# Kernel optimization log

Hardware: AMD Instinct MI355X
Metric: run time of the kernel (lower is better)

## Reference

```python
import jax, jax.numpy as jnp
import numpy as np
from functools import partial

B, A_PER, FH, FW, STRIDE = 32, 9, 100, 100, 16
PRE_NMS = 1000
POST_NMS = 1000
NMS_THRESH = 0.7
SCORE_THRESH = 0.0
MIN_SIZE = 0.001
BBOX_CLIP = float(np.log(1000.0 / 16.0))  # torchvision decode clamp on dw, dh


def make_anchors():
    # 3 scales x 3 ratios = 9 base anchors, tiled over the stride-16 grid in (h, w, a) order
    scales = np.array([32.0, 64.0, 128.0])
    ratios = np.array([0.5, 1.0, 2.0])
    ws = (scales[:, None] / np.sqrt(ratios)[None, :]).reshape(-1)
    hs = (scales[:, None] * np.sqrt(ratios)[None, :]).reshape(-1)
    base = np.stack([-ws / 2, -hs / 2, ws / 2, hs / 2], axis=1)  # [9,4]
    sx = (np.arange(FW) + 0.5) * STRIDE
    sy = (np.arange(FH) + 0.5) * STRIDE
    gy, gx = np.meshgrid(sy, sx, indexing="ij")
    shifts = np.stack([gx, gy, gx, gy], axis=-1)  # [H,W,4]
    anc = shifts[:, :, None, :] + base[None, None, :, :]  # [H,W,9,4]
    return jnp.asarray(anc.reshape(-1, 4), dtype=jnp.float32)


def setup_inputs() -> dict:
    key = jax.random.key(0)
    k1, k2 = jax.random.split(key)
    objectness = jax.random.normal(k1, (B, A_PER, FH, FW), dtype=jnp.float32)
    bbox_deltas = jax.random.normal(k2, (B, 4 * A_PER, FH, FW), dtype=jnp.float32)
    anchors = make_anchors()  # [FH*FW*A_PER, 4]
    return {"objectness": objectness, "bbox_deltas": bbox_deltas,
            "anchors": anchors, "image_h": FH * STRIDE, "image_w": FW * STRIDE}


def _flatten_head(cls, deltas):
    # cls: [B, A, H, W] (C=1); deltas: [B, 4A, H, W] -> (h, w, a) anchor order
    b, a, h, w = cls.shape
    obj = cls.transpose(0, 2, 3, 1).reshape(b, -1)                      # [B, HW*A]
    d = deltas.reshape(b, a, 4, h, w).transpose(0, 3, 4, 1, 2).reshape(b, -1, 4)
    return obj, d


def _decode(deltas, anchors):
    aw = anchors[:, 2] - anchors[:, 0]
    ah = anchors[:, 3] - anchors[:, 1]
    acx = anchors[:, 0] + 0.5 * aw
    acy = anchors[:, 1] + 0.5 * ah
    dx, dy = deltas[..., 0], deltas[..., 1]
    dw = jnp.minimum(deltas[..., 2], BBOX_CLIP)
    dh = jnp.minimum(deltas[..., 3], BBOX_CLIP)
    pcx = dx * aw + acx
    pcy = dy * ah + acy
    pw = jnp.exp(dw) * aw
    ph = jnp.exp(dh) * ah
    return jnp.stack([pcx - 0.5 * pw, pcy - 0.5 * ph,
                      pcx + 0.5 * pw, pcy + 0.5 * ph], axis=-1)


def _box_iou(a, b):
    area_a = (a[:, 2] - a[:, 0]) * (a[:, 3] - a[:, 1])
    area_b = (b[:, 2] - b[:, 0]) * (b[:, 3] - b[:, 1])
    lt = jnp.maximum(a[:, None, :2], b[None, :, :2])
    rb = jnp.minimum(a[:, None, 2:], b[None, :, 2:])
    wh = jnp.maximum(rb - lt, 0.0)
    inter = wh[..., 0] * wh[..., 1]
    return inter / (area_a[:, None] + area_b[None, :] - inter + 1e-12)


def _nms_keep(boxes, valid):
    # greedy NMS over score-sorted boxes; `valid` pre-masks small/low-score boxes
    k = boxes.shape[0]
    iou = _box_iou(boxes, boxes)
    ar = jnp.arange(k)

    def body(i, keep):
        sup = (iou[i] > NMS_THRESH) & keep[i] & (ar > i)
        return keep & jnp.logical_not(sup)

    return jax.lax.fori_loop(0, k, body, valid)


def _filter_one(boxes, logits, img_h, img_w):
    # boxes: [A,4], logits: [A]; per-image top-k -> clip -> filters -> NMS -> post top-k
    scores, idx = jax.lax.top_k(logits, PRE_NMS)     # sorted descending
    boxes = boxes[idx]
    prob = jax.nn.sigmoid(jax.lax.stop_gradient(scores))  # objectness is detached in filter_proposals
    x1 = jnp.clip(boxes[:, 0], 0.0, float(img_w))
    y1 = jnp.clip(boxes[:, 1], 0.0, float(img_h))
    x2 = jnp.clip(boxes[:, 2], 0.0, float(img_w))
    y2 = jnp.clip(boxes[:, 3], 0.0, float(img_h))
    boxes = jnp.stack([x1, y1, x2, y2], axis=-1)
    ws = boxes[:, 2] - boxes[:, 0]
    hs = boxes[:, 3] - boxes[:, 1]
    valid = (ws >= MIN_SIZE) & (hs >= MIN_SIZE) & (prob >= SCORE_THRESH)
    keep = jax.lax.stop_gradient(_nms_keep(boxes, valid))
    order = jnp.argsort(jnp.where(keep, 0, 1))[:POST_NMS]  # stable: kept boxes first, score order
    m = keep[order]
    out_boxes = jnp.where(m[:, None], boxes[order], 0.0)
    out_prob = jnp.where(m, prob[order], 0.0)
    return out_boxes, out_prob, m


def reference(objectness, bbox_deltas, anchors, image_h, image_w):
    obj, d = _flatten_head(objectness, bbox_deltas)      # [B, A_tot], [B, A_tot, 4]
    proposals = _decode(d, anchors)                      # [B, A_tot, 4]
    f = partial(_filter_one, img_h=image_h, img_w=image_w)
    boxes, prob, mask = jax.vmap(f)(proposals, obj)      # [B, POST_NMS, 4], [B, POST_NMS], [B, POST_NMS]
    return boxes, prob, mask
```

## Files before the change

kernel.cpp:

```cpp
#include <hip/hip_runtime.h>
#include <math.h>

#define BATCH 32
#define A_PER 9
#define FH 100
#define FW 100
#define A_TOT (FH*FW*A_PER)
#define KSEL 1000
#define BUFCAP 2048
#define NBIN 4096
#define NMS_T 0.7f
#define MIN_SZ 0.001f
#define BBOX_CLIP_F 4.135166556742356f

__device__ __forceinline__ unsigned int f2key(float f) {
    unsigned int u = __float_as_uint(f);
    return u ^ ((u & 0x80000000u) ? 0xFFFFFFFFu : 0x80000000u);
}
__device__ __forceinline__ float key2f(unsigned int k) {
    return __uint_as_float((k & 0x80000000u) ? (k ^ 0x80000000u) : ~k);
}

__global__ __launch_bounds__(256) void zero_kernel(
    uint4* __restrict__ ghist4, uint4* __restrict__ gcand4,
    uint4* __restrict__ gcnt4, uint4* __restrict__ valid4)
{
    const uint4 z = make_uint4(0u, 0u, 0u, 0u);
    int bid = blockIdx.x;
    if (bid < 128) {
        ghist4[bid * 256 + threadIdx.x] = z;
    } else if (bid < 256) {
        gcand4[(bid - 128) * 256 + threadIdx.x] = z;
    } else if (bid == 256) {
        if (threadIdx.x < 8) gcnt4[threadIdx.x] = z;
    } else {
        valid4[threadIdx.x] = z;
    }
}

__global__ __launch_bounds__(256) void hist_kernel(
    const float* __restrict__ obj, unsigned int* __restrict__ ghist)
{
    const int b = blockIdx.x >> 4;
    const int part = blockIdx.x & 15;
    const int tid = threadIdx.x;
    __shared__ unsigned int h[NBIN];
    for (int i = tid; i < NBIN; i += 256) h[i] = 0u;
    __syncthreads();
    const float4* sc4 = (const float4*)(obj + (size_t)b * A_TOT);
    for (int i = part * 256 + tid; i < A_TOT / 4; i += 4096) {
        float4 v = sc4[i];
        atomicAdd(&h[f2key(v.x) >> 20], 1u);
        atomicAdd(&h[f2key(v.y) >> 20], 1u);
        atomicAdd(&h[f2key(v.z) >> 20], 1u);
        atomicAdd(&h[f2key(v.w) >> 20], 1u);
    }
    __syncthreads();
    unsigned int* gh = ghist + (size_t)b * NBIN;
    for (int i = tid; i < NBIN; i += 256)
        if (h[i]) atomicAdd(&gh[i], h[i]);
}

__global__ __launch_bounds__(1024) void gather_kernel(
    const float* __restrict__ obj, const unsigned int* __restrict__ ghist,
    unsigned long long* __restrict__ gcand, unsigned int* __restrict__ gcnt)
{
    const int b = blockIdx.x >> 3;
    const int part = blockIdx.x & 7;
    const int tid = threadIdx.x;
    const int lane = tid & 63;
    const int wv = tid >> 6;

    __shared__ unsigned int wsum[16];
    __shared__ unsigned int sh_T, lcnt, base_sh;
    __shared__ unsigned long long cbuf[BUFCAP];

    if (tid == 0) lcnt = 0u;

    const unsigned int* gh = ghist + (size_t)b * NBIN;
    unsigned int h0 = gh[tid * 4 + 0], h1 = gh[tid * 4 + 1];
    unsigned int h2 = gh[tid * 4 + 2], h3 = gh[tid * 4 + 3];
    unsigned int ts = h0 + h1 + h2 + h3;
    unsigned int x = ts;
#pragma unroll
    for (int off = 1; off < 64; off <<= 1) {
        unsigned int v = __shfl_down(x, off);
        if (lane + off < 64) x += v;
    }
    if (lane == 0) wsum[wv] = x;
    __syncthreads();
    unsigned int swave = 0;
    for (int q = wv + 1; q < 16; ++q) swave += wsum[q];
    unsigned int S_hi = swave + (x - ts);
    unsigned int a3 = S_hi;
    unsigned int a2 = a3 + h3;
    unsigned int a1 = a2 + h2;
    unsigned int a0 = a1 + h1;
    if (a3 < KSEL && a3 + h3 >= KSEL) sh_T = (unsigned)(tid * 4 + 3);
    if (a2 < KSEL && a2 + h2 >= KSEL) sh_T = (unsigned)(tid * 4 + 2);
    if (a1 < KSEL && a1 + h1 >= KSEL) sh_T = (unsigned)(tid * 4 + 1);
    if (a0 < KSEL && a0 + h0 >= KSEL) sh_T = (unsigned)(tid * 4 + 0);
    __syncthreads();
    unsigned int T = sh_T;

    const float4* sc4 = (const float4*)(obj + (size_t)b * A_TOT);
#pragma unroll
    for (int j = 0; j < 3; ++j) {
        int i4 = j * 8192 + part * 1024 + tid;
        if (i4 < A_TOT / 4) {
            float4 v = sc4[i4];
            float vs[4] = {v.x, v.y, v.z, v.w};
#pragma unroll
            for (int c = 0; c < 4; ++c) {
                unsigned int key = f2key(vs[c]);
                if ((key >> 20) >= T) {
                    unsigned int pos = atomicAdd(&lcnt, 1u);
                    if (pos < BUFCAP) {
                        int e = i4 * 4 + c;
                        int a = e / 10000; int rem = e - a * 10000;
                        unsigned int i = (unsigned int)(rem * 9 + a);
                        cbuf[pos] = ((unsigned long long)key << 32) | (unsigned int)(~i);
                    }
                }
            }
        }
    }
    __syncthreads();
    if (tid == 0) base_sh = atomicAdd(&gcnt[b], lcnt);
    __syncthreads();
    unsigned int base = base_sh, n = lcnt;
    for (unsigned int i = tid; i < n; i += 1024) {
        unsigned int p = base + i;
        if (p < BUFCAP) gcand[(size_t)b * BUFCAP + p] = cbuf[i];
    }
}

__global__ __launch_bounds__(256) void rank_decode_kernel(
    const float* __restrict__ deltas,
    const float* __restrict__ anchors,
    const int* __restrict__ imh_p, const int* __restrict__ imw_p,
    const unsigned long long* __restrict__ gcand,
    const unsigned int* __restrict__ gcnt,
    float* __restrict__ boxes_ws, float* __restrict__ prob_ws,
    unsigned long long* __restrict__ valid_ws)
{
    const int b = blockIdx.x >> 3;
    const int part = blockIdx.x & 7;
    const int tid = threadIdx.x;
    const int lane = tid & 63;

    unsigned int cnt = gcnt[b]; if (cnt > BUFCAP) cnt = BUFCAP;
    const unsigned long long* gc = gcand + (size_t)b * BUFCAP;
    const int c = part * 256 + tid;
    unsigned long long my = gc[c];
    bool active = (c < (int)cnt);

    unsigned int ntile = (cnt + 63u) >> 6;
    unsigned int rank = 0;
    for (unsigned int t0 = 0; t0 < ntile; ++t0) {
        unsigned long long kk = gc[t0 * 64 + lane];
        unsigned int lo = (unsigned int)kk, hi = (unsigned int)(kk >> 32);
#pragma unroll
        for (int t = 0; t < 64; ++t) {
            unsigned int khi = __builtin_amdgcn_readlane(hi, t);
            unsigned int klo = __builtin_amdgcn_readlane(lo, t);
            unsigned long long kj = ((unsigned long long)khi << 32) | klo;
            rank += (kj > my) ? 1u : 0u;
        }
    }

    if (active && rank < KSEL) {
        unsigned int keyhi = (unsigned int)(my >> 32);
        unsigned int i = ~((unsigned int)my);
        float score = key2f(keyhi);
        float prob = 1.0f / (1.0f + expf(-score));

        int a = (int)(i % 9u); int hw = (int)(i / 9u);
        int h = hw / 100, w = hw - 100 * (hw / 100);
        const float* D = deltas + (size_t)b * 36 * 10000;
        int off = h * 100 + w;
        float dx  = D[(a * 4 + 0) * 10000 + off];
        float dy  = D[(a * 4 + 1) * 10000 + off];
        float dwv = fminf(D[(a * 4 + 2) * 10000 + off], BBOX_CLIP_F);
        float dhv = fminf(D[(a * 4 + 3) * 10000 + off], BBOX_CLIP_F);
        const float* anc = anchors + (size_t)i * 4;
        float ax1 = anc[0], ay1 = anc[1], ax2 = anc[2], ay2 = anc[3];
        float aw = ax2 - ax1, ah = ay2 - ay1;
        float acx = ax1 + 0.5f * aw, acy = ay1 + 0.5f * ah;
        float pcx = dx * aw + acx, pcy = dy * ah + acy;
        float pw = expf(dwv) * aw, ph = expf(dhv) * ah;
        float imw = (float)(*imw_p);
        float imh = (float)(*imh_p);
        float x1 = pcx - 0.5f * pw, y1 = pcy - 0.5f * ph;
        float x2 = pcx + 0.5f * pw, y2 = pcy + 0.5f * ph;
        x1 = fminf(fmaxf(x1, 0.0f), imw);
        y1 = fminf(fmaxf(y1, 0.0f), imh);
        x2 = fminf(fmaxf(x2, 0.0f), imw);
        y2 = fminf(fmaxf(y2, 0.0f), imh);
        bool valid = ((x2 - x1) >= MIN_SZ) && ((y2 - y1) >= MIN_SZ) && (prob >= 0.0f);
        ((float4*)boxes_ws)[(size_t)b * KSEL + rank] = make_float4(x1, y1, x2, y2);
        prob_ws[(size_t)b * KSEL + rank] = prob;
        if (valid)
            atomicOr(&valid_ws[b * 16 + (rank >> 6)], 1ull << (rank & 63));
    }
}

__global__ __launch_bounds__(1024) void mask_kernel(
    const float* __restrict__ boxes_ws, unsigned long long* __restrict__ mask_ws)
{
    const int b = blockIdx.x >> 3;
    const int part = blockIdx.x & 7;
    const int tid = threadIdx.x;
    const int lane = tid & 63;
    const int wv = tid >> 6;
    __shared__ float4 bx[KSEL];
    __shared__ float ar[KSEL];
    for (int r = tid; r < KSEL; r += 1024) {
        float4 v = ((const float4*)boxes_ws)[(size_t)b * KSEL + r];
        bx[r] = v;
        ar[r] = (v.z - v.x) * (v.w - v.y);
    }
    __syncthreads();
    int slot = part * 16 + wv;
    for (int r = slot; r < KSEL; r += 128) {
        float4 a = bx[r];
        float area_a = ar[r];
        unsigned long long* row = mask_ws + ((size_t)b * KSEL + r) * 16;
        int wlo = r >> 6;
        for (int t = 0; t < 16; ++t) {
            if (t < wlo) { if (lane == 0) row[t] = 0ull; continue; }
            int j = (t << 6) | lane;
            bool bit = false;
            if (j > r && j < KSEL) {
                float4 c = bx[j];
                float xx1 = fmaxf(a.x, c.x), yy1 = fmaxf(a.y, c.y);
                float xx2 = fminf(a.z, c.z), yy2 = fminf(a.w, c.w);
                float iw = fmaxf(xx2 - xx1, 0.0f), ih = fmaxf(yy2 - yy1, 0.0f);
                float inter = iw * ih;
                float iou = inter / (area_a + ar[j] - inter + 1e-12f);
                bit = iou > NMS_T;
            }
            unsigned long long m = __ballot(bit ? 1 : 0);
            if (lane == 0) row[t] = m;
        }
    }
}

__global__ __launch_bounds__(1024) void nms_out_kernel(
    const float* __restrict__ boxes_ws, const float* __restrict__ prob_ws,
    const unsigned long long* __restrict__ valid_ws,
    const unsigned long long* __restrict__ mask_ws,
    float* __restrict__ out)
{
    const int b = blockIdx.x;
    const int tid = threadIdx.x;
    const int lane = tid & 63;
    const int wv = tid >> 6;

    __shared__ unsigned long long partial[16];
    __shared__ unsigned long long keepw_sh[16];
    __shared__ unsigned int psum[16];
    __shared__ int klist[1024];
    __shared__ int cnt_sh;

    const unsigned long long* M = mask_ws + (size_t)b * KSEL * 16;

    unsigned long long Dd[16];
    unsigned long long validw = 0ull;
    if (wv == 0) {
#pragma unroll
        for (int w = 0; w < 16; ++w) {
            int row = w * 64 + lane;
            Dd[w] = (row < KSEL) ? M[(size_t)row * 16 + w] : 0ull;
        }
        validw = (lane < 16) ? valid_ws[b * 16 + lane] : 0ull;
    }
    if (tid == 0) { cnt_sh = 0; klist[0] = 0; }
    __syncthreads();

#pragma unroll
    for (int w = 0; w < 16; ++w) {
        int cnt = cnt_sh;
        int j = wv * 64 + lane;
        int jj = (j < cnt) ? j : 0;
        int kidx = klist[jj];
        unsigned long long v = M[(size_t)kidx * 16 + w];
        if (j >= cnt) v = 0ull;
#pragma unroll
        for (int off = 32; off > 0; off >>= 1) v |= __shfl_xor(v, off);
        if (lane == 0) partial[wv] = v;
        __syncthreads();

        if (wv == 0) {
            unsigned long long sup = (lane < 16) ? partial[lane] : 0ull;
#pragma unroll
            for (int off = 32; off > 0; off >>= 1) sup |= __shfl_xor(sup, off);
            unsigned long long cw = __shfl(validw, w) & ~sup;
            unsigned long long Dw = Dd[w];
            unsigned long long keptw = 0ull;
            while (cw) {
                unsigned long long myrow = Dw & cw;
                unsigned long long confl =
                    __ballot((((cw >> lane) & 1ull) && myrow != 0ull) ? 1 : 0);
                if (confl == 0ull) { keptw |= cw; break; }
                int c = __ffsll((long long)confl) - 1;
                unsigned long long le = (c == 63) ? ~0ull : ((1ull << (c + 1)) - 1ull);
                keptw |= cw & le;
                unsigned long long Dc = __shfl(Dw, c);
                cw &= ~le & ~Dc;
            }
            if ((keptw >> lane) & 1ull) {
                int rank = (int)__popcll(keptw & ((1ull << lane) - 1ull));
                klist[cnt + rank] = w * 64 + lane;
            }
            if (lane == 0) {
                keepw_sh[w] = keptw;
                cnt_sh = cnt + (int)__popcll(keptw);
            }
        }
        __syncthreads();
    }

    if (tid == 0) {
        unsigned int s = 0;
        for (int wq = 0; wq < 16; ++wq) { psum[wq] = s; s += __popcll(keepw_sh[wq]); }
    }
    __syncthreads();

    float* ob = out;
    float* op = out + (size_t)BATCH * KSEL * 4;
    float* om = op + (size_t)BATCH * KSEL;
    float* obb = ob + (size_t)b * KSEL * 4;
    float* opb = op + (size_t)b * KSEL;
    float* omb = om + (size_t)b * KSEL;

    for (int r = tid; r < KSEL; r += 1024) {
        obb[r * 4 + 0] = 0.0f; obb[r * 4 + 1] = 0.0f;
        obb[r * 4 + 2] = 0.0f; obb[r * 4 + 3] = 0.0f;
        opb[r] = 0.0f; omb[r] = 0.0f;
    }
    __syncthreads();
    for (int r = tid; r < KSEL; r += 1024) {
        unsigned long long kw = keepw_sh[r >> 6];
        if ((kw >> (r & 63)) & 1ull) {
            unsigned int p = psum[r >> 6] + (unsigned int)__popcll(kw & ((1ull << (r & 63)) - 1ull));
            size_t src = ((size_t)b * KSEL + r) * 4;
            obb[p * 4 + 0] = boxes_ws[src + 0];
            obb[p * 4 + 1] = boxes_ws[src + 1];
            obb[p * 4 + 2] = boxes_ws[src + 2];
            obb[p * 4 + 3] = boxes_ws[src + 3];
            opb[p] = prob_ws[(size_t)b * KSEL + r];
            omb[p] = 1.0f;
        }
    }
}

extern "C" void kernel_launch(void* const* d_in, const int* in_sizes, int n_in,
                              void* d_out, int out_size, void* d_ws, size_t ws_size,
                              hipStream_t stream) {
    const float* obj     = (const float*)d_in[0];
    const float* deltas  = (const float*)d_in[1];
    const float* anchors = (const float*)d_in[2];
    const int*   imh     = (const int*)d_in[3];
    const int*   imw     = (const int*)d_in[4];
    float* out = (float*)d_out;

    char* ws = (char*)d_ws;
    float* boxes_ws = (float*)ws;
    float* prob_ws  = (float*)(ws + 512000);
    unsigned long long* valid_ws = (unsigned long long*)(ws + 640000);
    unsigned long long* mask_ws  = (unsigned long long*)(ws + 644096);
    unsigned int* ghist = (unsigned int*)(ws + 644096);
    unsigned long long* gcand = (unsigned long long*)(ws + 1168384);
    unsigned int* gcnt  = (unsigned int*)(ws + 1692672);

    zero_kernel<<<258, 256, 0, stream>>>((uint4*)ghist, (uint4*)gcand,
                                         (uint4*)gcnt, (uint4*)valid_ws);
    hist_kernel<<<BATCH * 16, 256, 0, stream>>>(obj, ghist);
    gather_kernel<<<BATCH * 8, 1024, 0, stream>>>(obj, ghist, gcand, gcnt);
    rank_decode_kernel<<<BATCH * 8, 256, 0, stream>>>(deltas, anchors, imh, imw,
                                                      gcand, gcnt, boxes_ws, prob_ws, valid_ws);
    mask_kernel<<<BATCH * 8, 1024, 0, stream>>>(boxes_ws, mask_ws);
    nms_out_kernel<<<BATCH, 1024, 0, stream>>>(boxes_ws, prob_ws, valid_ws, mask_ws, out);
}
```

Before: 175.9 us.

## Fuse rank, decode, IoU mask and NMS into one per-image kernel

Removes the zero kernel by writing per-partition histograms and candidate lists that need no atomics or clearing. Rank, decode, IoU mask and NMS are merged into a single block per image that keeps boxes in shared memory. Suppression masks are now built lazily: only the diagonal 64x64 blocks are precomputed, and later words are suppressed by testing only against newly kept boxes. This cuts launches and global traffic for the full 1000x1000 mask, but leaves only 32 blocks doing the rank and NMS work and serialises more of it.

```diff
diff --git a/kernel.cpp b/kernel.cpp
--- a/kernel.cpp
+++ b/kernel.cpp
@@ -7,8 +7,10 @@
 #define FW 100
 #define A_TOT (FH*FW*A_PER)
 #define KSEL 1000
-#define BUFCAP 2048
 #define NBIN 4096
+#define NPART 8
+#define PCAP 512
+#define CCAP 2048
 #define NMS_T 0.7f
 #define MIN_SZ 0.001f
 #define BBOX_CLIP_F 4.135166556742356f
@@ -21,34 +23,17 @@
     return __uint_as_float((k & 0x80000000u) ? (k ^ 0x80000000u) : ~k);
 }
 
-__global__ __launch_bounds__(256) void zero_kernel(
-    uint4* __restrict__ ghist4, uint4* __restrict__ gcand4,
-    uint4* __restrict__ gcnt4, uint4* __restrict__ valid4)
+__global__ __launch_bounds__(256) void hist_kernel(
+    const float* __restrict__ obj, unsigned int* __restrict__ ghist_p)
 {
-    const uint4 z = make_uint4(0u, 0u, 0u, 0u);
-    int bid = blockIdx.x;
-    if (bid < 128) {
-        ghist4[bid * 256 + threadIdx.x] = z;
-    } else if (bid < 256) {
-        gcand4[(bid - 128) * 256 + threadIdx.x] = z;
-    } else if (bid == 256) {
-        if (threadIdx.x < 8) gcnt4[threadIdx.x] = z;
-    } else {
-        valid4[threadIdx.x] = z;
-    }
-}
-
-__global__ __launch_bounds__(256) void hist_kernel(
-    const float* __restrict__ obj, unsigned int* __restrict__ ghist)
-{
-    const int b = blockIdx.x >> 4;
-    const int part = blockIdx.x & 15;
+    const int b = blockIdx.x >> 3;
+    const int part = blockIdx.x & 7;
     const int tid = threadIdx.x;
     __shared__ unsigned int h[NBIN];
     for (int i = tid; i < NBIN; i += 256) h[i] = 0u;
     __syncthreads();
     const float4* sc4 = (const float4*)(obj + (size_t)b * A_TOT);
-    for (int i = part * 256 + tid; i < A_TOT / 4; i += 4096) {
+    for (int i = part * 256 + tid; i < A_TOT / 4; i += 2048) {
         float4 v = sc4[i];
         atomicAdd(&h[f2key(v.x) >> 20], 1u);
         atomicAdd(&h[f2key(v.y) >> 20], 1u);
@@ -56,14 +41,13 @@
         atomicAdd(&h[f2key(v.w) >> 20], 1u);
     }
     __syncthreads();
-    unsigned int* gh = ghist + (size_t)b * NBIN;
-    for (int i = tid; i < NBIN; i += 256)
-        if (h[i]) atomicAdd(&gh[i], h[i]);
+    unsigned int* gh = ghist_p + ((size_t)(b * NPART + part)) * NBIN;
+    for (int i = tid; i < NBIN; i += 256) gh[i] = h[i];
 }
 
 __global__ __launch_bounds__(1024) void gather_kernel(
-    const float* __restrict__ obj, const unsigned int* __restrict__ ghist,
-    unsigned long long* __restrict__ gcand, unsigned int* __restrict__ gcnt)
+    const float* __restrict__ obj, const unsigned int* __restrict__ ghist_p,
+    unsigned long long* __restrict__ pcand, unsigned int* __restrict__ pcnt)
 {
     const int b = blockIdx.x >> 3;
     const int part = blockIdx.x & 7;
@@ -72,14 +56,18 @@
     const int wv = tid >> 6;
 
     __shared__ unsigned int wsum[16];
-    __shared__ unsigned int sh_T, lcnt, base_sh;
-    __shared__ unsigned long long cbuf[BUFCAP];
+    __shared__ unsigned int sh_T, lcnt;
+    __shared__ unsigned long long cbuf[PCAP];
 
     if (tid == 0) lcnt = 0u;
 
-    const unsigned int* gh = ghist + (size_t)b * NBIN;
-    unsigned int h0 = gh[tid * 4 + 0], h1 = gh[tid * 4 + 1];
-    unsigned int h2 = gh[tid * 4 + 2], h3 = gh[tid * 4 + 3];
+    const unsigned int* gh = ghist_p + (size_t)b * NPART * NBIN;
+    unsigned int h0 = 0, h1 = 0, h2 = 0, h3 = 0;
+#pragma unroll
+    for (int p = 0; p < NPART; ++p) {
+        uint4 v = ((const uint4*)(gh + p * NBIN))[tid];
+        h0 += v.x; h1 += v.y; h2 += v.z; h3 += v.w;
+    }
     unsigned int ts = h0 + h1 + h2 + h3;
     unsigned int x = ts;
 #pragma unroll
@@ -115,7 +103,7 @@
                 unsigned int key = f2key(vs[c]);
                 if ((key >> 20) >= T) {
                     unsigned int pos = atomicAdd(&lcnt, 1u);
-                    if (pos < BUFCAP) {
+                    if (pos < PCAP) {
                         int e = i4 * 4 + c;
                         int a = e / 10000; int rem = e - a * 10000;
                         unsigned int i = (unsigned int)(rem * 9 + a);
@@ -126,130 +114,18 @@
         }
     }
     __syncthreads();
-    if (tid == 0) base_sh = atomicAdd(&gcnt[b], lcnt);
-    __syncthreads();
-    unsigned int base = base_sh, n = lcnt;
-    for (unsigned int i = tid; i < n; i += 1024) {
-        unsigned int p = base + i;
-        if (p < BUFCAP) gcand[(size_t)b * BUFCAP + p] = cbuf[i];
-    }
-}
-
-__global__ __launch_bounds__(256) void rank_decode_kernel(
+    unsigned int n = lcnt; if (n > PCAP) n = PCAP;
+    if (tid == 0) pcnt[b * NPART + part] = n;
+    unsigned long long* pc = pcand + (size_t)(b * NPART + part) * PCAP;
+    for (unsigned int i = tid; i < n; i += 1024) pc[i] = cbuf[i];
+}
+
+__global__ __launch_bounds__(1024) void mega_kernel(
     const float* __restrict__ deltas,
     const float* __restrict__ anchors,
     const int* __restrict__ imh_p, const int* __restrict__ imw_p,
-    const unsigned long long* __restrict__ gcand,
-    const unsigned int* __restrict__ gcnt,
-    float* __restrict__ boxes_ws, float* __restrict__ prob_ws,
-    unsigned long long* __restrict__ valid_ws)
-{
-    const int b = blockIdx.x >> 3;
-    const int part = blockIdx.x & 7;
-    const int tid = threadIdx.x;
-    const int lane = tid & 63;
-
-    unsigned int cnt = gcnt[b]; if (cnt > BUFCAP) cnt = BUFCAP;
-    const unsigned long long* gc = gcand + (size_t)b * BUFCAP;
-    const int c = part * 256 + tid;
-    unsigned long long my = gc[c];
-    bool active = (c < (int)cnt);
-
-    unsigned int ntile = (cnt + 63u) >> 6;
-    unsigned int rank = 0;
-    for (unsigned int t0 = 0; t0 < ntile; ++t0) {
-        unsigned long long kk = gc[t0 * 64 + lane];
-        unsigned int lo = (unsigned int)kk, hi = (unsigned int)(kk >> 32);
-#pragma unroll
-        for (int t = 0; t < 64; ++t) {
-            unsigned int khi = __builtin_amdgcn_readlane(hi, t);
-            unsigned int klo = __builtin_amdgcn_readlane(lo, t);
-            unsigned long long kj = ((unsigned long long)khi << 32) | klo;
-            rank += (kj > my) ? 1u : 0u;
-        }
-    }
-
-    if (active && rank < KSEL) {
-        unsigned int keyhi = (unsigned int)(my >> 32);
-        unsigned int i = ~((unsigned int)my);
-        float score = key2f(keyhi);
-        float prob = 1.0f / (1.0f + expf(-score));
-
-        int a = (int)(i % 9u); int hw = (int)(i / 9u);
-        int h = hw / 100, w = hw - 100 * (hw / 100);
-        const float* D = deltas + (size_t)b * 36 * 10000;
-        int off = h * 100 + w;
-        float dx  = D[(a * 4 + 0) * 10000 + off];
-        float dy  = D[(a * 4 + 1) * 10000 + off];
-        float dwv = fminf(D[(a * 4 + 2) * 10000 + off], BBOX_CLIP_F);
-        float dhv = fminf(D[(a * 4 + 3) * 10000 + off], BBOX_CLIP_F);
-        const float* anc = anchors + (size_t)i * 4;
-        float ax1 = anc[0], ay1 = anc[1], ax2 = anc[2], ay2 = anc[3];
-        float aw = ax2 - ax1, ah = ay2 - ay1;
-        float acx = ax1 + 0.5f * aw, acy = ay1 + 0.5f * ah;
-        float pcx = dx * aw + acx, pcy = dy * ah + acy;
-        float pw = expf(dwv) * aw, ph = expf(dhv) * ah;
-        float imw = (float)(*imw_p);
-        float imh = (float)(*imh_p);
-        float x1 = pcx - 0.5f * pw, y1 = pcy - 0.5f * ph;
-        float x2 = pcx + 0.5f * pw, y2 = pcy + 0.5f * ph;
-        x1 = fminf(fmaxf(x1, 0.0f), imw);
-        y1 = fminf(fmaxf(y1, 0.0f), imh);
-        x2 = fminf(fmaxf(x2, 0.0f), imw);
-        y2 = fminf(fmaxf(y2, 0.0f), imh);
-        bool valid = ((x2 - x1) >= MIN_SZ) && ((y2 - y1) >= MIN_SZ) && (prob >= 0.0f);
-        ((float4*)boxes_ws)[(size_t)b * KSEL + rank] = make_float4(x1, y1, x2, y2);
-        prob_ws[(size_t)b * KSEL + rank] = prob;
-        if (valid)
-            atomicOr(&valid_ws[b * 16 + (rank >> 6)], 1ull << (rank & 63));
-    }
-}
-
-__global__ __launch_bounds__(1024) void mask_kernel(
-    const float* __restrict__ boxes_ws, unsigned long long* __restrict__ mask_ws)
-{
-    const int b = blockIdx.x >> 3;
-    const int part = blockIdx.x & 7;
-    const int tid = threadIdx.x;
-    const int lane = tid & 63;
-    const int wv = tid >> 6;
-    __shared__ float4 bx[KSEL];
-    __shared__ float ar[KSEL];
-    for (int r = tid; r < KSEL; r += 1024) {
-        float4 v = ((const float4*)boxes_ws)[(size_t)b * KSEL + r];
-        bx[r] = v;
-        ar[r] = (v.z - v.x) * (v.w - v.y);
-    }
-    __syncthreads();
-    int slot = part * 16 + wv;
-    for (int r = slot; r < KSEL; r += 128) {
-        float4 a = bx[r];
-        float area_a = ar[r];
-        unsigned long long* row = mask_ws + ((size_t)b * KSEL + r) * 16;
-        int wlo = r >> 6;
-        for (int t = 0; t < 16; ++t) {
-            if (t < wlo) { if (lane == 0) row[t] = 0ull; continue; }
-            int j = (t << 6) | lane;
-            bool bit = false;
-            if (j > r && j < KSEL) {
-                float4 c = bx[j];
-                float xx1 = fmaxf(a.x, c.x), yy1 = fmaxf(a.y, c.y);
-                float xx2 = fminf(a.z, c.z), yy2 = fminf(a.w, c.w);
-                float iw = fmaxf(xx2 - xx1, 0.0f), ih = fmaxf(yy2 - yy1, 0.0f);
-                float inter = iw * ih;
-                float iou = inter / (area_a + ar[j] - inter + 1e-12f);
-                bit = iou > NMS_T;
-            }
-            unsigned long long m = __ballot(bit ? 1 : 0);
-            if (lane == 0) row[t] = m;
-        }
-    }
-}
-
-__global__ __launch_bounds__(1024) void nms_out_kernel(
-    const float* __restrict__ boxes_ws, const float* __restrict__ prob_ws,
-    const unsigned long long* __restrict__ valid_ws,
-    const unsigned long long* __restrict__ mask_ws,
+    const unsigned long long* __restrict__ pcand,
+    const unsigned int* __restrict__ pcnt,
     float* __restrict__ out)
 {
     const int b = blockIdx.x;
@@ -257,46 +133,126 @@
     const int lane = tid & 63;
     const int wv = tid >> 6;
 
-    __shared__ unsigned long long partial[16];
-    __shared__ unsigned long long keepw_sh[16];
+    __shared__ unsigned long long cand[CCAP];
+    __shared__ float4 bx[1024];
+    __shared__ float ar[1024];
+    __shared__ float prob_s[1024];
+    __shared__ unsigned long long Dd_s[1024];
+    __shared__ unsigned long long validw_s[16], supacc[16], keepw_sh[16];
+    __shared__ int klist[1024];
     __shared__ unsigned int psum[16];
-    __shared__ int klist[1024];
-    __shared__ int cnt_sh;
-
-    const unsigned long long* M = mask_ws + (size_t)b * KSEL * 16;
-
-    unsigned long long Dd[16];
-    unsigned long long validw = 0ull;
-    if (wv == 0) {
-#pragma unroll
-        for (int w = 0; w < 16; ++w) {
-            int row = w * 64 + lane;
-            Dd[w] = (row < KSEL) ? M[(size_t)row * 16 + w] : 0ull;
-        }
-        validw = (lane < 16) ? valid_ws[b * 16 + lane] : 0ull;
-    }
-    if (tid == 0) { cnt_sh = 0; klist[0] = 0; }
-    __syncthreads();
-
-#pragma unroll
+    __shared__ unsigned int segoff[NPART + 1];
+    __shared__ int cnt_sh, cold_sh;
+    __shared__ unsigned int cnt_cand;
+
+    if (tid == 0) {
+        unsigned int s = 0;
+        for (int p = 0; p < NPART; ++p) {
+            segoff[p] = s;
+            unsigned int c = pcnt[b * NPART + p];
+            if (c > PCAP) c = PCAP;
+            s += c;
+        }
+        segoff[NPART] = s;
+        cnt_cand = (s > CCAP) ? CCAP : s;
+        cnt_sh = 0; cold_sh = 0;
+    }
+    if (tid < 16) { validw_s[tid] = 0ull; supacc[tid] = 0ull; }
+    for (int i = tid; i < CCAP; i += 1024) cand[i] = 0ull;
+    __syncthreads();
+    for (int p = 0; p < NPART; ++p) {
+        unsigned int off = segoff[p];
+        unsigned int c = segoff[p + 1] - off;
+        const unsigned long long* pc = pcand + (size_t)(b * NPART + p) * PCAP;
+        for (unsigned int i = tid; i < c; i += 1024)
+            if (off + i < CCAP) cand[off + i] = pc[i];
+    }
+    __syncthreads();
+
+    unsigned int cnt = cnt_cand;
+    unsigned long long k0 = cand[tid];
+    unsigned long long k1 = cand[tid + 1024];
+    unsigned int ntile = (cnt + 63u) >> 6;
+    unsigned int rank0 = 0, rank1 = 0;
+    bool any1 = (cnt > 1024u);
+    for (unsigned int t0 = 0; t0 < ntile; ++t0) {
+        unsigned long long kk = cand[t0 * 64 + lane];
+        unsigned int lo = (unsigned int)kk, hi = (unsigned int)(kk >> 32);
+#pragma unroll
+        for (int t = 0; t < 64; ++t) {
+            unsigned int khi = __builtin_amdgcn_readlane(hi, t);
+            unsigned int klo = __builtin_amdgcn_readlane(lo, t);
+            unsigned long long kj = ((unsigned long long)khi << 32) | klo;
+            rank0 += (kj > k0) ? 1u : 0u;
+            if (any1) rank1 += (kj > k1) ? 1u : 0u;
+        }
+    }
+
+    float imw = (float)(*imw_p);
+    float imh = (float)(*imh_p);
+#pragma unroll
+    for (int s = 0; s < 2; ++s) {
+        int slot = tid + s * 1024;
+        unsigned long long my = (s == 0) ? k0 : k1;
+        unsigned int rk = (s == 0) ? rank0 : rank1;
+        if (slot < (int)cnt && rk < KSEL) {
+            unsigned int keyhi = (unsigned int)(my >> 32);
+            unsigned int i = ~((unsigned int)my);
+            float score = key2f(keyhi);
+            float prob = 1.0f / (1.0f + expf(-score));
+            int a = (int)(i % 9u); int hw = (int)(i / 9u);
+            int h = hw / 100, w = hw - 100 * (hw / 100);
+            const float* D = deltas + (size_t)b * 36 * 10000;
+            int off = h * 100 + w;
+            float dx  = D[(a * 4 + 0) * 10000 + off];
+            float dy  = D[(a * 4 + 1) * 10000 + off];
+            float dwv = fminf(D[(a * 4 + 2) * 10000 + off], BBOX_CLIP_F);
+            float dhv = fminf(D[(a * 4 + 3) * 10000 + off], BBOX_CLIP_F);
+            const float* anc = anchors + (size_t)i * 4;
+            float ax1 = anc[0], ay1 = anc[1], ax2 = anc[2], ay2 = anc[3];
+            float aw = ax2 - ax1, ah = ay2 - ay1;
+            float acx = ax1 + 0.5f * aw, acy = ay1 + 0.5f * ah;
+            float pcx = dx * aw + acx, pcy = dy * ah + acy;
+            float pw = expf(dwv) * aw, ph = expf(dhv) * ah;
+            float x1 = pcx - 0.5f * pw, y1 = pcy - 0.5f * ph;
+            float x2 = pcx + 0.5f * pw, y2 = pcy + 0.5f * ph;
+            x1 = fminf(fmaxf(x1, 0.0f), imw);
+            y1 = fminf(fmaxf(y1, 0.0f), imh);
+            x2 = fminf(fmaxf(x2, 0.0f), imw);
+            y2 = fminf(fmaxf(y2, 0.0f), imh);
+            bool valid = ((x2 - x1) >= MIN_SZ) && ((y2 - y1) >= MIN_SZ) && (prob >= 0.0f);
+            bx[rk] = make_float4(x1, y1, x2, y2);
+            ar[rk] = (x2 - x1) * (y2 - y1);
+            prob_s[rk] = prob;
+            if (valid) atomicOr(&validw_s[rk >> 6], 1ull << (rk & 63));
+        }
+    }
+    __syncthreads();
+
+    {
+        int r = wv * 64 + lane;
+        float4 a = bx[r]; float aa = ar[r];
+        unsigned long long row = 0ull;
+        if (r < KSEL) {
+            for (int t = 0; t < 64; ++t) {
+                int j2 = wv * 64 + t;
+                float4 c = bx[j2]; float ab = ar[j2];
+                float xx1 = fmaxf(a.x, c.x), yy1 = fmaxf(a.y, c.y);
+                float xx2 = fminf(a.z, c.z), yy2 = fminf(a.w, c.w);
+                float iw = fmaxf(xx2 - xx1, 0.0f), ih = fmaxf(yy2 - yy1, 0.0f);
+                float inter = iw * ih;
+                float iou = inter / (aa + ab - inter + 1e-12f);
+                if (t > lane && j2 < KSEL && iou > NMS_T) row |= (1ull << t);
+            }
+        }
+        Dd_s[wv * 64 + lane] = row;
+    }
+    __syncthreads();
+
     for (int w = 0; w < 16; ++w) {
-        int cnt = cnt_sh;
-        int j = wv * 64 + lane;
-        int jj = (j < cnt) ? j : 0;
-        int kidx = klist[jj];
-        unsigned long long v = M[(size_t)kidx * 16 + w];
-        if (j >= cnt) v = 0ull;
-#pragma unroll
-        for (int off = 32; off > 0; off >>= 1) v |= __shfl_xor(v, off);
-        if (lane == 0) partial[wv] = v;
-        __syncthreads();
-
         if (wv == 0) {
-            unsigned long long sup = (lane < 16) ? partial[lane] : 0ull;
-#pragma unroll
-            for (int off = 32; off > 0; off >>= 1) sup |= __shfl_xor(sup, off);
-            unsigned long long cw = __shfl(validw, w) & ~sup;
-            unsigned long long Dw = Dd[w];
+            unsigned long long cw = validw_s[w] & ~supacc[w];
+            unsigned long long Dw = Dd_s[w * 64 + lane];
             unsigned long long keptw = 0ull;
             while (cw) {
                 unsigned long long myrow = Dw & cw;
@@ -309,14 +265,41 @@
                 unsigned long long Dc = __shfl(Dw, c);
                 cw &= ~le & ~Dc;
             }
+            int cnt0 = cnt_sh;
             if ((keptw >> lane) & 1ull) {
-                int rank = (int)__popcll(keptw & ((1ull << lane) - 1ull));
-                klist[cnt + rank] = w * 64 + lane;
+                int rk = (int)__popcll(keptw & ((1ull << lane) - 1ull));
+                klist[cnt0 + rk] = w * 64 + lane;
             }
             if (lane == 0) {
                 keepw_sh[w] = keptw;
-                cnt_sh = cnt + (int)__popcll(keptw);
-            }
+                cold_sh = cnt0;
+                cnt_sh = cnt0 + (int)__popcll(keptw);
+            }
+        }
+        __syncthreads();
+        int tw = w + 1 + wv;
+        if (tw < 16) {
+            int c0 = cold_sh, c1 = cnt_sh;
+            int t2 = tw * 64 + lane;
+            float4 cbox = bx[t2]; float cab = ar[t2];
+            bool tval = (t2 < KSEL);
+            unsigned long long acc = 0ull;
+            for (int ii = c0; ii < c1; ++ii) {
+                int k = klist[ii];
+                float4 a = bx[k]; float aa = ar[k];
+                bool bit = false;
+                if (tval) {
+                    float xx1 = fmaxf(a.x, cbox.x), yy1 = fmaxf(a.y, cbox.y);
+                    float xx2 = fminf(a.z, cbox.z), yy2 = fminf(a.w, cbox.w);
+                    float iw = fmaxf(xx2 - xx1, 0.0f), ih = fmaxf(yy2 - yy1, 0.0f);
+                    float inter = iw * ih;
+                    float iou = inter / (aa + cab - inter + 1e-12f);
+                    bit = iou > NMS_T;
+                }
+                unsigned long long m = __ballot(bit ? 1 : 0);
+                acc |= m;
+            }
+            if (lane == 0) supacc[tw] |= acc;
         }
         __syncthreads();
     }
@@ -344,12 +327,12 @@
         unsigned long long kw = keepw_sh[r >> 6];
         if ((kw >> (r & 63)) & 1ull) {
             unsigned int p = psum[r >> 6] + (unsigned int)__popcll(kw & ((1ull << (r & 63)) - 1ull));
-            size_t src = ((size_t)b * KSEL + r) * 4;
-            obb[p * 4 + 0] = boxes_ws[src + 0];
-            obb[p * 4 + 1] = boxes_ws[src + 1];
-            obb[p * 4 + 2] = boxes_ws[src + 2];
-            obb[p * 4 + 3] = boxes_ws[src + 3];
-            opb[p] = prob_ws[(size_t)b * KSEL + r];
+            float4 v = bx[r];
+            obb[p * 4 + 0] = v.x;
+            obb[p * 4 + 1] = v.y;
+            obb[p * 4 + 2] = v.z;
+            obb[p * 4 + 3] = v.w;
+            opb[p] = prob_s[r];
             omb[p] = 1.0f;
         }
     }
@@ -366,20 +349,12 @@
     float* out = (float*)d_out;
 
     char* ws = (char*)d_ws;
-    float* boxes_ws = (float*)ws;
-    float* prob_ws  = (float*)(ws + 512000);
-    unsigned long long* valid_ws = (unsigned long long*)(ws + 640000);
-    unsigned long long* mask_ws  = (unsigned long long*)(ws + 644096);
-    unsigned int* ghist = (unsigned int*)(ws + 644096);
-    unsigned long long* gcand = (unsigned long long*)(ws + 1168384);
-    unsigned int* gcnt  = (unsigned int*)(ws + 1692672);
-
-    zero_kernel<<<258, 256, 0, stream>>>((uint4*)ghist, (uint4*)gcand,
-                                         (uint4*)gcnt, (uint4*)valid_ws);
-    hist_kernel<<<BATCH * 16, 256, 0, stream>>>(obj, ghist);
-    gather_kernel<<<BATCH * 8, 1024, 0, stream>>>(obj, ghist, gcand, gcnt);
-    rank_decode_kernel<<<BATCH * 8, 256, 0, stream>>>(deltas, anchors, imh, imw,
-                                                      gcand, gcnt, boxes_ws, prob_ws, valid_ws);
-    mask_kernel<<<BATCH * 8, 1024, 0, stream>>>(boxes_ws, mask_ws);
-    nms_out_kernel<<<BATCH, 1024, 0, stream>>>(boxes_ws, prob_ws, valid_ws, mask_ws, out);
-}
+    unsigned long long* pcand = (unsigned long long*)ws;
+    unsigned int* pcnt = (unsigned int*)(ws + 1048576);
+    unsigned int* ghist_p = (unsigned int*)(ws + 1049600);
+
+    hist_kernel<<<BATCH * NPART, 256, 0, stream>>>(obj, ghist_p);
+    gather_kernel<<<BATCH * NPART, 1024, 0, stream>>>(obj, ghist_p, pcand, pcnt);
+    mega_kernel<<<BATCH, 1024, 0, stream>>>(deltas, anchors, imh, imw,
+                                            pcand, pcnt, out);
+}
```

After: 370.2 us. 110% more time.
